# Optimization experiments

Measured on AMD Instinct MI355X. Metric: run time of the kernel, lower is better.

## Reference

```python
import jax, jax.numpy as jnp
import numpy as np

GROUPS = 8
EPS = 1e-5
NUM_HEADS = 8


def group_norm(x, gamma, beta):
    # x: [B, C, N]; GroupNorm over (C//G, N) per group, per sample (torch semantics)
    B, C, N = x.shape
    xg = x.reshape(B, GROUPS, (C // GROUPS) * N)
    mean = xg.mean(axis=-1, keepdims=True)
    var = xg.var(axis=-1, keepdims=True)
    xn = ((xg - mean) * jax.lax.rsqrt(var + EPS)).reshape(B, C, N)
    return xn * gamma[None, :, None] + beta[None, :, None]


def setup_inputs() -> dict:
    key = jax.random.key(0)
    ks = jax.random.split(key, 6)
    B, N, C = 4, 2048, 512
    s = 0.02
    return {
        "x": jax.random.normal(ks[0], (B, N, C), jnp.float32),
        "pe": jax.random.normal(ks[1], (B, N, C), jnp.float32),
        "qkv_w": jax.random.normal(ks[2], (3 * C, C), jnp.float32) * s,
        "proj_w": jax.random.normal(ks[3], (C, C), jnp.float32) * s,
        "proj_b": jnp.zeros((C,), jnp.float32),
        "conv1_w": jax.random.normal(ks[4], (C, C), jnp.float32) * s,
        "conv1_b": jnp.zeros((C,), jnp.float32),
        "gn1_g": jnp.ones((C,), jnp.float32),
        "gn1_b": jnp.zeros((C,), jnp.float32),
        "conv2_w": jax.random.normal(ks[5], (C, C), jnp.float32) * s,
        "conv2_b": jnp.zeros((C,), jnp.float32),
        "gn2_g": jnp.ones((C,), jnp.float32),
        "gn2_b": jnp.zeros((C,), jnp.float32),
    }


def reference(x, pe, qkv_w, proj_w, proj_b, conv1_w, conv1_b, gn1_g, gn1_b,
              conv2_w, conv2_b, gn2_g, gn2_b):
    B, N, C = x.shape
    H = NUM_HEADS
    D = C // H
    scale = D ** -0.5

    pe_t = pe.transpose(0, 2, 1)  # [B, C, N]
    # Conv1d(kernel=1) == per-position linear over channels
    p1 = group_norm(jnp.einsum('oc,bcn->bon', conv1_w, pe_t) + conv1_b[None, :, None], gn1_g, gn1_b)
    p2 = group_norm(jnp.einsum('oc,bcn->bon', conv2_w, pe_t) + conv2_b[None, :, None], gn2_g, gn2_b)
    pe_1 = p1.transpose(0, 2, 1)                 # [B, N, C]
    pe_attn = jax.nn.sigmoid(jnp.einsum('bnc,bcm->bnm', pe_1, p2))  # [B, N, N]

    qkv = (x @ qkv_w.T).reshape(B, N, 3, H, D).transpose(2, 0, 3, 1, 4)  # [3, B, H, N, D]
    q, k, v = qkv[0], qkv[1], qkv[2]

    attn = jnp.einsum('bhnd,bhmd->bhnm', q, k) * scale
    attn = attn * pe_attn[:, None, :, :]
    attn = jax.nn.softmax(attn, axis=-1)

    out = jnp.einsum('bhnm,bhmd->bhnd', attn, v)          # [B, H, N, D]
    out = out.transpose(0, 2, 1, 3).reshape(B, N, C)
    return out @ proj_w.T + proj_b
```

## Files before the change

kernel.cpp:

```cpp
#include <hip/hip_runtime.h>
#include <hip/hip_bf16.h>

typedef __attribute__((ext_vector_type(8))) short bf16x8;
typedef __attribute__((ext_vector_type(4))) float f32x4;

__device__ __forceinline__ float bfu2f(unsigned int u) {
    return __uint_as_float(u << 16);
}
__device__ __forceinline__ unsigned short f2bfu(float f) {
    unsigned int u = __float_as_uint(f);
    u += 0x7fffu + ((u >> 16) & 1u);
    return (unsigned short)(u >> 16);
}

__global__ __launch_bounds__(256) void cvt_all(
    const float* __restrict__ x, unsigned short* __restrict__ xb,
    const float* __restrict__ pe, unsigned short* __restrict__ peb,
    const float* __restrict__ w0, unsigned short* __restrict__ d0,
    const float* __restrict__ w1, unsigned short* __restrict__ d1,
    const float* __restrict__ w2, unsigned short* __restrict__ d2,
    const float* __restrict__ w3, unsigned short* __restrict__ d3,
    const float* __restrict__ c1bias, const float* __restrict__ c2bias,
    float* __restrict__ biasws) {
    const int tid = threadIdx.x;
    if (blockIdx.x == 0) {
        if (tid < 128) ((float4*)biasws)[tid] = ((const float4*)c1bias)[tid];
        else ((float4*)biasws)[tid] = ((const float4*)c2bias)[tid - 128];
    }
    int i = blockIdx.x * 256 + tid;
    const int stride = gridDim.x * 256;
    for (; i < 1441792; i += stride) {
        if (i < 1048576) {
            float4 v = reinterpret_cast<const float4*>(x)[i];
            ushort4 o;
            o.x = f2bfu(v.x); o.y = f2bfu(v.y); o.z = f2bfu(v.z); o.w = f2bfu(v.w);
            reinterpret_cast<ushort4*>(xb)[i] = o;
            float4 u = reinterpret_cast<const float4*>(pe)[i];
            ushort4 p;
            p.x = f2bfu(u.x); p.y = f2bfu(u.y); p.z = f2bfu(u.z); p.w = f2bfu(u.w);
            reinterpret_cast<ushort4*>(peb)[i] = p;
        } else {
            int j = i - 1048576;
            const float* s; unsigned short* d;
            if (j < 196608)      { s = w0; d = d0; }
            else if (j < 262144) { s = w1; d = d1; j -= 196608; }
            else if (j < 327680) { s = w2; d = d2; j -= 262144; }
            else                 { s = w3; d = d3; j -= 327680; }
            float4 v = reinterpret_cast<const float4*>(s)[j];
            ushort4 o;
            o.x = f2bfu(v.x); o.y = f2bfu(v.y); o.z = f2bfu(v.z); o.w = f2bfu(v.w);
            reinterpret_cast<ushort4*>(d)[j] = o;
        }
    }
}

template <int EPI>
__global__ __launch_bounds__(256) void gemm_nt(
    const unsigned short* __restrict__ A, const unsigned short* __restrict__ B,
    void* __restrict__ C0, void* __restrict__ C1, void* __restrict__ C2,
    const float* __restrict__ bias, int K, long sA, long sB, long sC,
    int nx, int ny) {
    __shared__ unsigned short As[2][128 * 32];
    __shared__ unsigned short Bs[2][128 * 32];
    int lin = blockIdx.x;
    const int qsw = gridDim.x >> 3;
    lin = (lin & 7) * qsw + (lin >> 3);
    const int bx = lin % nx;
    const int t2 = lin / nx;
    const int by = t2 % ny;
    const int bz = t2 / ny;
    const int tid = threadIdx.x;
    const int l = tid & 63, w = tid >> 6;
    const int wr = w >> 1, wc = w & 1, lr = l & 15, lh = l >> 4;
    const int m0 = by * 128, n0 = bx * 128;
    A += (size_t)bz * sA;
    B += (size_t)bz * sB;
    f32x4 acc[4][4] = {};

    const int srow = l >> 2, sslot = l & 3;
    auto stage = [&](int bufi, int k0) {
#pragma unroll
        for (int i = 0; i < 2; i++) {
            const int row = w * 32 + i * 16 + srow;
            const int cs = (sslot ^ (row & 3)) * 8;
            const int ldsoff = (w * 32 + i * 16) * 32;
            __builtin_amdgcn_global_load_lds(
                (const __attribute__((address_space(1))) void*)(A + (size_t)(m0 + row) * K + k0 + cs),
                (__attribute__((address_space(3))) void*)&As[bufi][ldsoff], 16, 0, 0);
            __builtin_amdgcn_global_load_lds(
                (const __attribute__((address_space(1))) void*)(B + (size_t)(n0 + row) * K + k0 + cs),
                (__attribute__((address_space(3))) void*)&Bs[bufi][ldsoff], 16, 0, 0);
        }
    };

    const int nks = K >> 5;
    stage(0, 0);
    asm volatile("s_waitcnt vmcnt(0)" ::: "memory");
    __builtin_amdgcn_s_barrier();
    __builtin_amdgcn_sched_barrier(0);

    const int colA = (lh ^ (lr & 3)) << 3;
    for (int ks = 0; ks < nks; ks++) {
        const int cur = ks & 1;
        if (ks + 1 < nks) stage(cur ^ 1, (ks + 1) << 5);
        bf16x8 af[4], bfr[4];
#pragma unroll
        for (int i = 0; i < 4; i++)
            af[i] = *reinterpret_cast<const bf16x8*>(&As[cur][(wr * 64 + i * 16 + lr) * 32 + colA]);
#pragma unroll
        for (int i = 0; i < 4; i++)
            bfr[i] = *reinterpret_cast<const bf16x8*>(&Bs[cur][(wc * 64 + i * 16 + lr) * 32 + colA]);
        __builtin_amdgcn_s_setprio(1);
#pragma unroll
        for (int mi = 0; mi < 4; mi++)
#pragma unroll
            for (int ni = 0; ni < 4; ni++)
                acc[mi][ni] = __builtin_amdgcn_mfma_f32_16x16x32_bf16(af[mi], bfr[ni], acc[mi][ni], 0, 0, 0);
        __builtin_amdgcn_s_setprio(0);
        if (ks + 1 < nks) {
            asm volatile("s_waitcnt vmcnt(0) lgkmcnt(0)" ::: "memory");
            __builtin_amdgcn_s_barrier();
            __builtin_amdgcn_sched_barrier(0);
        }
    }

    float sgn = 0.f, qgn = 0.f;
#pragma unroll
    for (int mi = 0; mi < 4; mi++) {
#pragma unroll
        for (int ni = 0; ni < 4; ni++) {
#pragma unroll
            for (int r = 0; r < 4; r++) {
                const int row = m0 + wr * 64 + mi * 16 + lh * 4 + r;
                const int col = n0 + wc * 64 + ni * 16 + lr;
                float v = acc[mi][ni][r];
                if constexpr (EPI == 0) {
                    v += bias[bz * 512 + col];
                    sgn += v; qgn += v * v;
                    ((unsigned short*)C0)[(size_t)bz * sC + (size_t)row * 512 + col] = f2bfu(v);
                } else if constexpr (EPI == 1) {
                    const int part = col >> 9, hh = (col >> 6) & 7, d = col & 63;
                    const int b = row >> 11, n = row & 2047;
                    const size_t bh = (size_t)(b * 8 + hh);
                    if (part == 0)
                        ((unsigned short*)C0)[(bh * 2048 + n) * 64 + d] = f2bfu(v * 0.1803368801111244f);
                    else if (part == 1)
                        ((unsigned short*)C1)[(bh * 2048 + n) * 64 + d] = f2bfu(v);
                    else
                        ((unsigned short*)C2)[(bh * 64 + d) * 2048 + n] = f2bfu(v);
                } else if constexpr (EPI == 2) {
                    const float sg = 1.0f / (1.0f + __expf(-v));
                    ((unsigned short*)C0)[(size_t)bz * sC + (size_t)row * 2048 + col] = f2bfu(sg);
                } else {
                    ((float*)C0)[(size_t)row * 512 + col] = v + bias[col];
                }
            }
        }
    }
    if constexpr (EPI == 0) {
#pragma unroll
        for (int s = 1; s < 64; s <<= 1) {
            sgn += __shfl_xor(sgn, s);
            qgn += __shfl_xor(qgn, s);
        }
        if (l == 0) {
            const int bg = ((by >> 4) << 3) + bx * 2 + wc;
            float* part = (float*)C1;
            atomicAdd(&part[(bz * 32 + bg) * 2 + 0], sgn);
            atomicAdd(&part[(bz * 32 + bg) * 2 + 1], qgn);
        }
    }
}

__global__ __launch_bounds__(256) void gn_apply(unsigned short* __restrict__ c1,
                                                unsigned short* __restrict__ c2,
                                                const float* __restrict__ part,
                                                const float* __restrict__ g1, const float* __restrict__ b1,
                                                const float* __restrict__ g2, const float* __restrict__ b2) {
    __shared__ float sst[2][32][2];
    const int tid = threadIdx.x;
    if (tid < 64) {
        const int z = tid >> 5, bg = tid & 31;
        const float S = part[(z * 32 + bg) * 2 + 0];
        const float Q = part[(z * 32 + bg) * 2 + 1];
        const float inv = 1.0f / 131072.0f;
        const float m = S * inv;
        const float v = fmaxf(Q * inv - m * m, 0.f);
        sst[z][bg][0] = m;
        sst[z][bg][1] = rsqrtf(v + 1e-5f);
    }
    __syncthreads();
    int i = blockIdx.x * 256 + tid;
    const int stride = gridDim.x * 256;
    for (; i < 524288; i += stride) {
        const size_t e = (size_t)i * 8;
        const int b = (int)(e >> 20);
        const int o = (int)(e & 511);
        const int g = o >> 6;
        const int bg = (b << 3) + g;
        const float m1 = sst[0][bg][0], r1 = sst[0][bg][1];
        const float m2 = sst[1][bg][0], r2 = sst[1][bg][1];
        uint4 v1 = *reinterpret_cast<const uint4*>(c1 + e);
        uint4 v2 = *reinterpret_cast<const uint4*>(c2 + e);
        unsigned int a1[4] = {v1.x, v1.y, v1.z, v1.w};
        unsigned int a2[4] = {v2.x, v2.y, v2.z, v2.w};
        unsigned int o1[4], o2[4];
#pragma unroll
        for (int j = 0; j < 4; j++) {
            const int oo = o + j * 2;
            float x0 = (bfu2f(a1[j] & 0xffffu) - m1) * r1 * g1[oo] + b1[oo];
            float x1 = (bfu2f(a1[j] >> 16) - m1) * r1 * g1[oo + 1] + b1[oo + 1];
            o1[j] = (unsigned int)f2bfu(x0) | ((unsigned int)f2bfu(x1) << 16);
            float y0 = (bfu2f(a2[j] & 0xffffu) - m2) * r2 * g2[oo] + b2[oo];
            float y1 = (bfu2f(a2[j] >> 16) - m2) * r2 * g2[oo + 1] + b2[oo + 1];
            o2[j] = (unsigned int)f2bfu(y0) | ((unsigned int)f2bfu(y1) << 16);
        }
        uint4 w1; w1.x = o1[0]; w1.y = o1[1]; w1.z = o1[2]; w1.w = o1[3];
        uint4 w2; w2.x = o2[0]; w2.y = o2[1]; w2.z = o2[2]; w2.w = o2[3];
        *reinterpret_cast<uint4*>(c1 + e) = w1;
        *reinterpret_cast<uint4*>(c2 + e) = w2;
    }
}

__global__ __launch_bounds__(512, 4) void attn_fused(
    const unsigned short* __restrict__ qb, const unsigned short* __restrict__ kb,
    const unsigned short* __restrict__ vT, const unsigned short* __restrict__ pea,
    unsigned short* __restrict__ hbuf) {
    __shared__ unsigned short Ks[2][64 * 64];
    __shared__ unsigned short Vs[2][64 * 64];
    __shared__ unsigned short Pl[8][16 * 64];
    const int tid = threadIdx.x, l = tid & 63, w = tid >> 6;
    const int lr = l & 15, lh = l >> 4;
    const int bid = blockIdx.x;
    const int h = bid >> 6, rst = bid & 63, nt = rst & 15, b = rst >> 4;
    const size_t bh = (size_t)(b * 8 + h);
    const unsigned short* qp = qb + bh * 2048 * 64;
    const unsigned short* kp = kb + bh * 2048 * 64;
    const unsigned short* vp = vT + bh * 64 * 2048;
    const unsigned short* pep = pea + (size_t)b * 2048 * 2048;
    const int qrow = nt * 128 + 16 * w + lr;

    bf16x8 qf[2];
    qf[0] = *reinterpret_cast<const bf16x8*>(qp + (size_t)qrow * 64 + lh * 8);
    qf[1] = *reinterpret_cast<const bf16x8*>(qp + (size_t)qrow * 64 + 32 + lh * 8);

    const int swz = (lr & 7) << 4;
    const int colK0 = ((16 * lh) ^ swz) >> 1;
    const int colK1 = ((64 + 16 * lh) ^ swz) >> 1;

    const unsigned short* perp = pep + (size_t)qrow * 2048;
    uint2 peR[4];
#pragma unroll
    for (int mf = 0; mf < 4; mf++)
        peR[mf] = *reinterpret_cast<const uint2*>(perp + 16 * mf + 4 * lh);

    f32x4 oacc[4] = {};
    float mrun = -1e30f, lrun = 0.f;

    const int srow = l >> 3, sslot = l & 7;
    auto stage_kv = [&](int bufi, int m0) {
        const int row = w * 8 + srow;
        const int cs = (sslot ^ srow) * 8;
        const int ldsoff = w * 512;
        __builtin_amdgcn_global_load_lds(
            (const __attribute__((address_space(1))) void*)(kp + (size_t)(m0 + row) * 64 + cs),
            (__attribute__((address_space(3))) void*)&Ks[bufi][ldsoff], 16, 0, 0);
        __builtin_amdgcn_global_load_lds(
            (const __attribute__((address_space(1))) void*)(vp + (size_t)row * 2048 + m0 + cs),
            (__attribute__((address_space(3))) void*)&Vs[bufi][ldsoff], 16, 0, 0);
    };

    stage_kv(0, 0);
    asm volatile("s_waitcnt vmcnt(0)" ::: "memory");
    __builtin_amdgcn_s_barrier();
    __builtin_amdgcn_sched_barrier(0);

    for (int mt = 0; mt < 32; mt++) {
        const int cur = mt & 1;
        if (mt + 1 < 32) stage_kv(cur ^ 1, (mt + 1) * 64);
        const unsigned short* Kb = Ks[cur];
        const unsigned short* Vb = Vs[cur];

        f32x4 st[4] = {};
        __builtin_amdgcn_s_setprio(1);
#pragma unroll
        for (int mf = 0; mf < 4; mf++) {
            bf16x8 kf0 = *reinterpret_cast<const bf16x8*>(&Kb[(mf * 16 + lr) * 64 + colK0]);
            bf16x8 kf1 = *reinterpret_cast<const bf16x8*>(&Kb[(mf * 16 + lr) * 64 + colK1]);
            st[mf] = __builtin_amdgcn_mfma_f32_16x16x32_bf16(kf0, qf[0], st[mf], 0, 0, 0);
            st[mf] = __builtin_amdgcn_mfma_f32_16x16x32_bf16(kf1, qf[1], st[mf], 0, 0, 0);
        }
        __builtin_amdgcn_s_setprio(0);

        float p[4][4];
#pragma unroll
        for (int mf = 0; mf < 4; mf++) {
            p[mf][0] = st[mf][0] * bfu2f(peR[mf].x & 0xffffu);
            p[mf][1] = st[mf][1] * bfu2f(peR[mf].x >> 16);
            p[mf][2] = st[mf][2] * bfu2f(peR[mf].y & 0xffffu);
            p[mf][3] = st[mf][3] * bfu2f(peR[mf].y >> 16);
        }
        uint2 peN[4];
        if (mt + 1 < 32) {
            const unsigned short* pn = perp + (mt + 1) * 64;
#pragma unroll
            for (int mf = 0; mf < 4; mf++)
                peN[mf] = *reinterpret_cast<const uint2*>(pn + 16 * mf + 4 * lh);
        }
        float pm = fmaxf(p[0][0], p[0][1]);
        pm = fmaxf(fmaxf(pm, p[0][2]), p[0][3]);
#pragma unroll
        for (int mf = 1; mf < 4; mf++) {
            pm = fmaxf(fmaxf(pm, p[mf][0]), p[mf][1]);
            pm = fmaxf(fmaxf(pm, p[mf][2]), p[mf][3]);
        }
        pm = fmaxf(pm, __shfl_xor(pm, 16));
        pm = fmaxf(pm, __shfl_xor(pm, 32));
        if (__any(pm > mrun + 11.5416f)) {
            const float mnew = fmaxf(mrun, pm);
            const float fac = __builtin_amdgcn_exp2f(mrun - mnew);
            lrun *= fac;
#pragma unroll
            for (int df = 0; df < 4; df++)
#pragma unroll
                for (int r = 0; r < 4; r++) oacc[df][r] *= fac;
            mrun = mnew;
        }
        float ss = 0.f;
        unsigned int pk[8];
#pragma unroll
        for (int mf = 0; mf < 4; mf++) {
#pragma unroll
            for (int t = 0; t < 2; t++) {
                const float a = __builtin_amdgcn_exp2f(p[mf][2 * t] - mrun);
                const float c = __builtin_amdgcn_exp2f(p[mf][2 * t + 1] - mrun);
                unsigned int pkv;
                asm("v_cvt_pk_bf16_f32 %0, %1, %2" : "=v"(pkv) : "v"(a), "v"(c));
                pk[mf * 2 + t] = pkv;
                ss += a + c;
            }
        }
        ss += __shfl_xor(ss, 16);
        ss += __shfl_xor(ss, 32);
        lrun += ss;
        unsigned short* PlW = Pl[w];
        const int plswz = (lr & 7) << 4;
#pragma unroll
        for (int mf = 0; mf < 4; mf++)
#pragma unroll
            for (int t = 0; t < 2; t++) {
                const int cb = (mf * 32 + lh * 8 + 4 * t) ^ plswz;
                *reinterpret_cast<unsigned int*>(&PlW[lr * 64 + (cb >> 1)]) = pk[mf * 2 + t];
            }
        bf16x8 pb0 = *reinterpret_cast<const bf16x8*>(&PlW[lr * 64 + (((lh * 16) ^ plswz) >> 1)]);
        bf16x8 pb1 = *reinterpret_cast<const bf16x8*>(&PlW[lr * 64 + (((64 + lh * 16) ^ plswz) >> 1)]);
        __builtin_amdgcn_s_setprio(1);
#pragma unroll
        for (int df = 0; df < 4; df++) {
            bf16x8 vf0 = *reinterpret_cast<const bf16x8*>(&Vb[(df * 16 + lr) * 64 + colK0]);
            bf16x8 vf1 = *reinterpret_cast<const bf16x8*>(&Vb[(df * 16 + lr) * 64 + colK1]);
            oacc[df] = __builtin_amdgcn_mfma_f32_16x16x32_bf16(vf0, pb0, oacc[df], 0, 0, 0);
            oacc[df] = __builtin_amdgcn_mfma_f32_16x16x32_bf16(vf1, pb1, oacc[df], 0, 0, 0);
        }
        __builtin_amdgcn_s_setprio(0);
        if (mt + 1 < 32) {
            asm volatile("s_waitcnt vmcnt(0) lgkmcnt(0)" ::: "memory");
            __builtin_amdgcn_s_barrier();
            __builtin_amdgcn_sched_barrier(0);
#pragma unroll
            for (int mf = 0; mf < 4; mf++) peR[mf] = peN[mf];
        }
    }
    const float inv = 1.0f / lrun;
    const size_t base = ((size_t)b * 2048 + qrow) * 512 + h * 64;
#pragma unroll
    for (int df = 0; df < 4; df++) {
#pragma unroll
        for (int t = 0; t < 2; t++) {
            const unsigned int ua = f2bfu(oacc[df][2 * t] * inv);
            const unsigned int uc = f2bfu(oacc[df][2 * t + 1] * inv);
            *reinterpret_cast<unsigned int*>(&hbuf[base + 16 * df + 4 * lh + 2 * t]) = ua | (uc << 16);
        }
    }
}

extern "C" void kernel_launch(void* const* d_in, const int* in_sizes, int n_in,
                              void* d_out, int out_size, void* d_ws, size_t ws_size,
                              hipStream_t stream) {
    const float* x       = (const float*)d_in[0];
    const float* pe      = (const float*)d_in[1];
    const float* qkv_w   = (const float*)d_in[2];
    const float* proj_w  = (const float*)d_in[3];
    const float* proj_b  = (const float*)d_in[4];
    const float* conv1_w = (const float*)d_in[5];
    const float* conv1_b = (const float*)d_in[6];
    const float* gn1_g   = (const float*)d_in[7];
    const float* gn1_b   = (const float*)d_in[8];
    const float* conv2_w = (const float*)d_in[9];
    const float* conv2_b = (const float*)d_in[10];
    const float* gn2_g   = (const float*)d_in[11];
    const float* gn2_b   = (const float*)d_in[12];
    float* out = (float*)d_out;

    char* ws = (char*)d_ws;
    size_t off = 0;
    auto alloc = [&](size_t bytes) -> void* {
        void* p = ws + off;
        off += (bytes + 255) & ~(size_t)255;
        return p;
    };
    unsigned short* xb     = (unsigned short*)alloc(8388608);
    unsigned short* peb    = (unsigned short*)alloc(8388608);
    unsigned short* qkvwb  = (unsigned short*)alloc(1572864);
    unsigned short* projwb = (unsigned short*)alloc(524288);
    unsigned short* w1b    = (unsigned short*)alloc(524288);
    unsigned short* w2b    = (unsigned short*)alloc(524288);
    unsigned short* c1b    = (unsigned short*)alloc(8388608);
    unsigned short* c2b    = (unsigned short*)alloc(8388608);
    unsigned short* qbuf   = (unsigned short*)alloc(8388608);
    unsigned short* kbuf   = (unsigned short*)alloc(8388608);
    unsigned short* vtb    = (unsigned short*)alloc(8388608);
    unsigned short* peatt  = (unsigned short*)alloc(33554432);
    unsigned short* hbuf   = (unsigned short*)alloc(8388608);
    float* part            = (float*)alloc(512);
    float* biasws          = (float*)alloc(4096);

    dim3 blk(256);
    hipMemsetAsync(part, 0, 512, stream);
    cvt_all<<<2048, blk, 0, stream>>>(x, xb, pe, peb, qkv_w, qkvwb, proj_w, projwb,
                                      conv1_w, w1b, conv2_w, w2b, conv1_b, conv2_b, biasws);

    gemm_nt<0><<<dim3(512), blk, 0, stream>>>(peb, w1b, c1b, part, nullptr, biasws,
                                              512, 0, 262144, 4194304, 4, 64);
    gn_apply<<<1024, blk, 0, stream>>>(c1b, c2b, part, gn1_g, gn1_b, gn2_g, gn2_b);
    gemm_nt<1><<<dim3(768), blk, 0, stream>>>(xb, qkvwb, qbuf, kbuf, vtb, nullptr,
                                              512, 0, 0, 0, 12, 64);
    gemm_nt<2><<<dim3(1024), blk, 0, stream>>>(c1b, c2b, peatt, nullptr, nullptr, nullptr,
                                               512, 1048576, 1048576, 4194304, 16, 16);
    attn_fused<<<dim3(512), dim3(512), 0, stream>>>(qbuf, kbuf, vtb, peatt, hbuf);
    gemm_nt<3><<<dim3(256), blk, 0, stream>>>(hbuf, projwb, out, nullptr, nullptr, proj_b,
                                              512, 0, 0, 0, 4, 64);
}
```

Measured before the change: 222.0 us.

## Double the KV tile to 128 keys per iteration in fused attention

The attention loop now processes 128 keys per iteration instead of 64, halving the iteration count and the number of barriers and online-softmax rescale checks. K/V shared-memory buffers double in size, with a new swizzled staging layout for the wider V rows, and the P tile is written and consumed in two halves through the same per-wave LDS scratch. The cost is higher register pressure (8 score fragments, 8 pe prefetch registers) and more LDS per block, which may reduce occupancy under the 512x4 launch bound.

```diff
diff --git a/kernel.cpp b/kernel.cpp
--- a/kernel.cpp
+++ b/kernel.cpp
@@ -226,8 +226,8 @@
     const unsigned short* __restrict__ qb, const unsigned short* __restrict__ kb,
     const unsigned short* __restrict__ vT, const unsigned short* __restrict__ pea,
     unsigned short* __restrict__ hbuf) {
-    __shared__ unsigned short Ks[2][64 * 64];
-    __shared__ unsigned short Vs[2][64 * 64];
+    __shared__ unsigned short Ks[2][128 * 64];
+    __shared__ unsigned short Vs[2][64 * 128];
     __shared__ unsigned short Pl[8][16 * 64];
     const int tid = threadIdx.x, l = tid & 63, w = tid >> 6;
     const int lr = l & 15, lh = l >> 4;
@@ -247,27 +247,34 @@
     const int swz = (lr & 7) << 4;
     const int colK0 = ((16 * lh) ^ swz) >> 1;
     const int colK1 = ((64 + 16 * lh) ^ swz) >> 1;
+    int colV[4];
+#pragma unroll
+    for (int c = 0; c < 4; c++) colV[c] = ((64 * c + 16 * lh) ^ swz) >> 1;
 
     const unsigned short* perp = pep + (size_t)qrow * 2048;
-    uint2 peR[4];
-#pragma unroll
-    for (int mf = 0; mf < 4; mf++)
+    uint2 peR[8];
+#pragma unroll
+    for (int mf = 0; mf < 8; mf++)
         peR[mf] = *reinterpret_cast<const uint2*>(perp + 16 * mf + 4 * lh);
 
     f32x4 oacc[4] = {};
     float mrun = -1e30f, lrun = 0.f;
 
-    const int srow = l >> 3, sslot = l & 7;
     auto stage_kv = [&](int bufi, int m0) {
-        const int row = w * 8 + srow;
-        const int cs = (sslot ^ srow) * 8;
-        const int ldsoff = w * 512;
-        __builtin_amdgcn_global_load_lds(
-            (const __attribute__((address_space(1))) void*)(kp + (size_t)(m0 + row) * 64 + cs),
-            (__attribute__((address_space(3))) void*)&Ks[bufi][ldsoff], 16, 0, 0);
-        __builtin_amdgcn_global_load_lds(
-            (const __attribute__((address_space(1))) void*)(vp + (size_t)row * 2048 + m0 + cs),
-            (__attribute__((address_space(3))) void*)&Vs[bufi][ldsoff], 16, 0, 0);
+#pragma unroll
+        for (int i = 0; i < 2; i++) {
+            const int kc = w * 128 + i * 64 + l;
+            const int krow = kc >> 3, kslot = kc & 7;
+            const int kcs = (kslot ^ (krow & 7)) * 8;
+            __builtin_amdgcn_global_load_lds(
+                (const __attribute__((address_space(1))) void*)(kp + (size_t)(m0 + krow) * 64 + kcs),
+                (__attribute__((address_space(3))) void*)&Ks[bufi][(w * 128 + i * 64) * 8], 16, 0, 0);
+            const int vrow = kc >> 4, vslot = kc & 15;
+            const int vcs = (vslot ^ (vrow & 7)) * 8;
+            __builtin_amdgcn_global_load_lds(
+                (const __attribute__((address_space(1))) void*)(vp + (size_t)vrow * 2048 + m0 + vcs),
+                (__attribute__((address_space(3))) void*)&Vs[bufi][(w * 128 + i * 64) * 8], 16, 0, 0);
+        }
     };
 
     stage_kv(0, 0);
@@ -275,42 +282,43 @@
     __builtin_amdgcn_s_barrier();
     __builtin_amdgcn_sched_barrier(0);
 
-    for (int mt = 0; mt < 32; mt++) {
+    for (int mt = 0; mt < 16; mt++) {
         const int cur = mt & 1;
-        if (mt + 1 < 32) stage_kv(cur ^ 1, (mt + 1) * 64);
+        if (mt + 1 < 16) stage_kv(cur ^ 1, (mt + 1) * 128);
         const unsigned short* Kb = Ks[cur];
         const unsigned short* Vb = Vs[cur];
 
-        f32x4 st[4] = {};
+        f32x4 st[8];
         __builtin_amdgcn_s_setprio(1);
 #pragma unroll
-        for (int mf = 0; mf < 4; mf++) {
+        for (int mf = 0; mf < 8; mf++) {
+            f32x4 z = {};
             bf16x8 kf0 = *reinterpret_cast<const bf16x8*>(&Kb[(mf * 16 + lr) * 64 + colK0]);
             bf16x8 kf1 = *reinterpret_cast<const bf16x8*>(&Kb[(mf * 16 + lr) * 64 + colK1]);
-            st[mf] = __builtin_amdgcn_mfma_f32_16x16x32_bf16(kf0, qf[0], st[mf], 0, 0, 0);
-            st[mf] = __builtin_amdgcn_mfma_f32_16x16x32_bf16(kf1, qf[1], st[mf], 0, 0, 0);
+            z = __builtin_amdgcn_mfma_f32_16x16x32_bf16(kf0, qf[0], z, 0, 0, 0);
+            st[mf] = __builtin_amdgcn_mfma_f32_16x16x32_bf16(kf1, qf[1], z, 0, 0, 0);
         }
         __builtin_amdgcn_s_setprio(0);
 
-        float p[4][4];
-#pragma unroll
-        for (int mf = 0; mf < 4; mf++) {
+        float p[8][4];
+#pragma unroll
+        for (int mf = 0; mf < 8; mf++) {
             p[mf][0] = st[mf][0] * bfu2f(peR[mf].x & 0xffffu);
             p[mf][1] = st[mf][1] * bfu2f(peR[mf].x >> 16);
             p[mf][2] = st[mf][2] * bfu2f(peR[mf].y & 0xffffu);
             p[mf][3] = st[mf][3] * bfu2f(peR[mf].y >> 16);
         }
-        uint2 peN[4];
-        if (mt + 1 < 32) {
-            const unsigned short* pn = perp + (mt + 1) * 64;
-#pragma unroll
-            for (int mf = 0; mf < 4; mf++)
+        uint2 peN[8];
+        if (mt + 1 < 16) {
+            const unsigned short* pn = perp + (mt + 1) * 128;
+#pragma unroll
+            for (int mf = 0; mf < 8; mf++)
                 peN[mf] = *reinterpret_cast<const uint2*>(pn + 16 * mf + 4 * lh);
         }
         float pm = fmaxf(p[0][0], p[0][1]);
         pm = fmaxf(fmaxf(pm, p[0][2]), p[0][3]);
 #pragma unroll
-        for (int mf = 1; mf < 4; mf++) {
+        for (int mf = 1; mf < 8; mf++) {
             pm = fmaxf(fmaxf(pm, p[mf][0]), p[mf][1]);
             pm = fmaxf(fmaxf(pm, p[mf][2]), p[mf][3]);
         }
@@ -327,9 +335,9 @@
             mrun = mnew;
         }
         float ss = 0.f;
-        unsigned int pk[8];
-#pragma unroll
-        for (int mf = 0; mf < 4; mf++) {
+        unsigned int pk[16];
+#pragma unroll
+        for (int mf = 0; mf < 8; mf++) {
 #pragma unroll
             for (int t = 0; t < 2; t++) {
                 const float a = __builtin_amdgcn_exp2f(p[mf][2 * t] - mrun);
@@ -346,29 +354,32 @@
         unsigned short* PlW = Pl[w];
         const int plswz = (lr & 7) << 4;
 #pragma unroll
-        for (int mf = 0; mf < 4; mf++)
-#pragma unroll
-            for (int t = 0; t < 2; t++) {
-                const int cb = (mf * 32 + lh * 8 + 4 * t) ^ plswz;
-                *reinterpret_cast<unsigned int*>(&PlW[lr * 64 + (cb >> 1)]) = pk[mf * 2 + t];
+        for (int kh = 0; kh < 2; kh++) {
+#pragma unroll
+            for (int mq = 0; mq < 4; mq++)
+#pragma unroll
+                for (int t = 0; t < 2; t++) {
+                    const int cb = (mq * 32 + lh * 8 + 4 * t) ^ plswz;
+                    *reinterpret_cast<unsigned int*>(&PlW[lr * 64 + (cb >> 1)]) = pk[(kh * 4 + mq) * 2 + t];
+                }
+            bf16x8 pb0 = *reinterpret_cast<const bf16x8*>(&PlW[lr * 64 + (((lh * 16) ^ plswz) >> 1)]);
+            bf16x8 pb1 = *reinterpret_cast<const bf16x8*>(&PlW[lr * 64 + (((64 + lh * 16) ^ plswz) >> 1)]);
+            __builtin_amdgcn_s_setprio(1);
+#pragma unroll
+            for (int df = 0; df < 4; df++) {
+                bf16x8 vf0 = *reinterpret_cast<const bf16x8*>(&Vb[(df * 16 + lr) * 128 + colV[kh * 2]]);
+                bf16x8 vf1 = *reinterpret_cast<const bf16x8*>(&Vb[(df * 16 + lr) * 128 + colV[kh * 2 + 1]]);
+                oacc[df] = __builtin_amdgcn_mfma_f32_16x16x32_bf16(vf0, pb0, oacc[df], 0, 0, 0);
+                oacc[df] = __builtin_amdgcn_mfma_f32_16x16x32_bf16(vf1, pb1, oacc[df], 0, 0, 0);
             }
-        bf16x8 pb0 = *reinterpret_cast<const bf16x8*>(&PlW[lr * 64 + (((lh * 16) ^ plswz) >> 1)]);
-        bf16x8 pb1 = *reinterpret_cast<const bf16x8*>(&PlW[lr * 64 + (((64 + lh * 16) ^ plswz) >> 1)]);
-        __builtin_amdgcn_s_setprio(1);
-#pragma unroll
-        for (int df = 0; df < 4; df++) {
-            bf16x8 vf0 = *reinterpret_cast<const bf16x8*>(&Vb[(df * 16 + lr) * 64 + colK0]);
-            bf16x8 vf1 = *reinterpret_cast<const bf16x8*>(&Vb[(df * 16 + lr) * 64 + colK1]);
-            oacc[df] = __builtin_amdgcn_mfma_f32_16x16x32_bf16(vf0, pb0, oacc[df], 0, 0, 0);
-            oacc[df] = __builtin_amdgcn_mfma_f32_16x16x32_bf16(vf1, pb1, oacc[df], 0, 0, 0);
-        }
-        __builtin_amdgcn_s_setprio(0);
-        if (mt + 1 < 32) {
+            __builtin_amdgcn_s_setprio(0);
+        }
+        if (mt + 1 < 16) {
             asm volatile("s_waitcnt vmcnt(0) lgkmcnt(0)" ::: "memory");
             __builtin_amdgcn_s_barrier();
             __builtin_amdgcn_sched_barrier(0);
 #pragma unroll
-            for (int mf = 0; mf < 4; mf++) peR[mf] = peN[mf];
+            for (int mf = 0; mf < 8; mf++) peR[mf] = peN[mf];
         }
     }
     const float inv = 1.0f / lrun;
```

After: 221.7 us. No clear change (-0.1%).
